# Kernel optimization log

Measured on AMD Instinct MI355X. Metric: run time of the kernel, lower is better.

The kernel has to match this reference:

```python
import jax, jax.numpy as jnp
import numpy as np
import math

D_MODEL = 1024
NUM_HEADS = 16
HEAD_DIM = D_MODEL // NUM_HEADS
ROPE_BASE = 10000.0
ROTARY_DIM = HEAD_DIM - HEAD_DIM % 2  # 64


def setup_inputs() -> dict:
    key = jax.random.key(0)
    ks = jax.random.split(key, 6)
    B, T = 4, 2048
    tokens = jax.random.normal(ks[0], (B, T, D_MODEL), dtype=jnp.float32)
    padding_mask = jax.random.randint(ks[1], (B, T), 0, 2) == 1  # True = pad
    s = 1.0 / math.sqrt(D_MODEL)
    W_qkv = jax.random.normal(ks[2], (D_MODEL, 3 * D_MODEL), dtype=jnp.float32) * s
    b_qkv = jnp.zeros((3 * D_MODEL,), dtype=jnp.float32)
    W_out = jax.random.normal(ks[3], (D_MODEL, D_MODEL), dtype=jnp.float32) * s
    b_out = jnp.zeros((D_MODEL,), dtype=jnp.float32)
    return {"tokens": tokens, "padding_mask": padding_mask,
            "W_qkv": W_qkv, "b_qkv": b_qkv, "W_out": W_out, "b_out": b_out}


def _apply_rope(x):
    # x: [B, H, T, head_dim]; full head dim is rotary here (ROTARY_DIM == HEAD_DIM)
    T = x.shape[-2]
    pos = jnp.arange(T, dtype=jnp.float32)[:, None]                      # [T,1]
    freqs = jnp.exp(jnp.arange(0, ROTARY_DIM, 2, dtype=jnp.float32)
                    * (-math.log(ROPE_BASE) / ROTARY_DIM))               # [rd/2]
    ang = pos * freqs[None, :]                                           # [T, rd/2]
    sin = jnp.sin(ang)[None, None].astype(x.dtype)
    cos = jnp.cos(ang)[None, None].astype(x.dtype)
    rot = x[..., :ROTARY_DIM].reshape(*x.shape[:-1], ROTARY_DIM // 2, 2)
    even, odd = rot[..., 0], rot[..., 1]
    rotated = jnp.stack((even * cos - odd * sin, even * sin + odd * cos), axis=-1)
    rotated = rotated.reshape(*x.shape[:-1], ROTARY_DIM)
    return jnp.concatenate([rotated, x[..., ROTARY_DIM:]], axis=-1)


def _safe_key_padding_mask(padding_mask):
    # True = pad; if a row is fully padded, unmask it to avoid NaN softmax rows
    all_pad = jnp.all(padding_mask, axis=-1, keepdims=True)
    return jnp.where(all_pad, False, padding_mask)


def reference(tokens, padding_mask, W_qkv, b_qkv, W_out, b_out):
    B, T, _ = tokens.shape
    qkv = tokens @ W_qkv + b_qkv                                         # [B,T,3d]
    q, k, v = jnp.split(qkv, 3, axis=-1)
    def split_heads(x):
        return x.reshape(B, T, NUM_HEADS, HEAD_DIM).transpose(0, 2, 1, 3)
    q, k, v = split_heads(q), split_heads(k), split_heads(v)
    q = _apply_rope(q)
    k = _apply_rope(k)
    valid = ~_safe_key_padding_mask(padding_mask)                        # [B,T], True = attend
    scores = jnp.einsum('bhqd,bhkd->bhqk', q, k) / math.sqrt(HEAD_DIM)   # [B,H,T,T]
    neg = jnp.asarray(jnp.finfo(scores.dtype).min, scores.dtype)
    scores = jnp.where(valid[:, None, None, :], scores, neg)
    attn = jax.nn.softmax(scores, axis=-1)
    out = jnp.einsum('bhqk,bhkd->bhqd', attn, v)                         # [B,H,T,hd]
    out = out.transpose(0, 2, 1, 3).reshape(B, T, D_MODEL)
    return out @ W_out + b_out
```

## Files before the change

### kernel.cpp

```cpp
#include <hip/hip_runtime.h>
#include <cmath>

#define T_SEQ 2048
#define NH    16
#define HD    64
#define DM    1024
#define BATCH 4

typedef __attribute__((ext_vector_type(8))) short s16x8;
typedef __attribute__((ext_vector_type(8))) _Float16 f16x8;
typedef __attribute__((ext_vector_type(2))) __fp16 fp16v2;
typedef __attribute__((ext_vector_type(4))) float f32x4;
typedef unsigned short ushort_t;

__device__ __forceinline__ ushort_t f2h(float x) {
    union { _Float16 h; ushort_t u; } v; v.h = (_Float16)x; return v.u;
}
__device__ __forceinline__ float h2f(ushort_t u) {
    union { ushort_t u; _Float16 h; } v; v.u = u; return (float)v.h;
}
__device__ __forceinline__ float exp2_raw(float x) {
    return __builtin_amdgcn_exp2f(x);
}
__device__ __forceinline__ unsigned pkrtz(float a, float b) {
    union { fp16v2 h; unsigned u; } v;
    v.h = __builtin_amdgcn_cvt_pkrtz(a, b);
    return v.u;
}

__device__ __forceinline__ void dma16(const void* g, const void* l) {
    __builtin_amdgcn_global_load_lds(
        (const __attribute__((address_space(1))) unsigned int*)(unsigned long long)g,
        (__attribute__((address_space(3))) unsigned int*)(unsigned int)(unsigned long long)l,
        16, 0, 0);
}

__global__ void maskprep_kernel(const int* __restrict__ pad, float* __restrict__ valid)
{
    __shared__ int sall[256];
    const int b = blockIdx.x;
    const int t = threadIdx.x;
    int allp = 1;
    for (int i = t; i < T_SEQ; i += 256) allp &= (pad[b*T_SEQ + i] != 0) ? 1 : 0;
    sall[t] = allp;
    __syncthreads();
    for (int s = 128; s > 0; s >>= 1) {
        if (t < s) sall[t] &= sall[t + s];
        __syncthreads();
    }
    const int ap = sall[0];
    for (int i = t; i < T_SEQ; i += 256) {
        const int p = (pad[b*T_SEQ + i] != 0) ? 1 : 0;
        valid[b*T_SEQ + i] = (p && !ap) ? -1e30f : 0.0f;
    }
}

__global__ __launch_bounds__(256)
void transpose_split_kernel(const float* __restrict__ W,
                            ushort_t* __restrict__ Th, ushort_t* __restrict__ Tl,
                            int K, int N)
{
    __shared__ float T[64][68];
    const int tid = threadIdx.x;
    const int n0 = blockIdx.x * 64;
    const int k0 = blockIdx.y * 64;
#pragma unroll
    for (int i = 0; i < 4; ++i) {
        const int kr = (tid >> 4) + i*16;
        const int nc = (tid & 15) * 4;
        const float4 v = *(const float4*)&W[(size_t)(k0 + kr)*N + n0 + nc];
        T[nc+0][kr] = v.x; T[nc+1][kr] = v.y; T[nc+2][kr] = v.z; T[nc+3][kr] = v.w;
    }
    __syncthreads();
#pragma unroll
    for (int i = 0; i < 4; ++i) {
        const int nr = (tid >> 4) + i*16;
        const int kc = (tid & 15) * 4;
        ushort_t h[4], l[4];
#pragma unroll
        for (int j = 0; j < 4; ++j) {
            const float x = T[nr][kc + j] * 32.0f;
            h[j] = f2h(x);
            l[j] = f2h(x - h2f(h[j]));
        }
        const size_t off = (size_t)(n0 + nr)*K + k0 + kc;
        *(short4*)&Th[off] = make_short4((short)h[0], (short)h[1], (short)h[2], (short)h[3]);
        *(short4*)&Tl[off] = make_short4((short)l[0], (short)l[1], (short)l[2], (short)l[3]);
    }
}

__global__ __launch_bounds__(256)
void split_kernel(const float* __restrict__ X, ushort_t* __restrict__ H)
{
    const int i = blockIdx.x * 256 + threadIdx.x;
    const float4 v = ((const float4*)X)[i];
    *(short4*)&H[(size_t)i*4] = make_short4(
        (short)f2h(v.x), (short)f2h(v.y), (short)f2h(v.z), (short)f2h(v.w));
}

template<int EPI>
__global__ __launch_bounds__(256)
void mfma_gemm_kernel(const ushort_t* __restrict__ Atf,
                      const ushort_t* __restrict__ BTh, const ushort_t* __restrict__ BTl,
                      const float* __restrict__ bias,
                      float* __restrict__ O0,
                      ushort_t* __restrict__ Qf,
                      ushort_t* __restrict__ Khf,
                      ushort_t* __restrict__ Vthf,
                      int M, int N, int K)
{
    __shared__ __align__(16) char smem[34816];
    char* smA  = smem;
    char* smBh = smem + 4096;
    char* smBl = smem + 12288;

    const int tid  = threadIdx.x;
    const int w    = tid >> 6;
    const int ln   = tid & 63;
    const int lx   = ln & 15;
    const int quad = ln >> 4;
    const int mw   = (w >> 1) * 32;
    const int nw   = (w & 1) * 64;
    const int m0   = blockIdx.y * 64;
    const int n0   = blockIdx.x * 128;

    const int swc = ((ln & 3) ^ ((ln >> 3) & 3)) * 8;
    const size_t gaA = (size_t)(m0 + w*16 + (ln >> 2))*K + swc;
    const size_t gaB = (size_t)(n0 + w*32 + (ln >> 2))*K + swc;
    const int ldsA = (w*64 + ln)*16;
    const int ldsB = (w*128 + ln)*16;

#define ISSUE_DMA(kk) do {                                               \
        dma16(Atf + gaA + (kk),        smA  + ldsA);                     \
        dma16(BTh + gaB + (kk),        smBh + ldsB);                     \
        dma16(BTh + gaB + 16*K + (kk), smBh + ldsB + 1024);              \
        dma16(BTl + gaB + (kk),        smBl + ldsB);                     \
        dma16(BTl + gaB + 16*K + (kk), smBl + ldsB + 1024);              \
    } while (0)

    f32x4 acc[2][4];
#pragma unroll
    for (int mt = 0; mt < 2; ++mt)
#pragma unroll
        for (int nt = 0; nt < 4; ++nt) acc[mt][nt] = (f32x4){0.f,0.f,0.f,0.f};

    ISSUE_DMA(0);

    const int cs = (quad ^ ((lx >> 1) & 3)) * 16;

    for (int kk = 0; kk < K; kk += 32) {
        __syncthreads();

        f16x8 bfh[4], bfl[4];
#pragma unroll
        for (int nt = 0; nt < 4; ++nt) {
            const int off = (nw + nt*16 + lx)*64 + cs;
            bfh[nt] = *(const f16x8*)(smBh + off);
            bfl[nt] = *(const f16x8*)(smBl + off);
        }
        f16x8 af0, af1;
        {
            af0 = *(const f16x8*)(smA + (mw + lx)*64 + cs);
            af1 = *(const f16x8*)(smA + (mw + 16 + lx)*64 + cs);
        }
        __syncthreads();
        if (kk + 32 < K) ISSUE_DMA(kk + 32);

        __builtin_amdgcn_s_setprio(1);
#pragma unroll
        for (int nt = 0; nt < 4; ++nt) {
            acc[0][nt] = __builtin_amdgcn_mfma_f32_16x16x32_f16(af0, bfh[nt], acc[0][nt], 0, 0, 0);
            acc[0][nt] = __builtin_amdgcn_mfma_f32_16x16x32_f16(af0, bfl[nt], acc[0][nt], 0, 0, 0);
        }
#pragma unroll
        for (int nt = 0; nt < 4; ++nt) {
            acc[1][nt] = __builtin_amdgcn_mfma_f32_16x16x32_f16(af1, bfh[nt], acc[1][nt], 0, 0, 0);
            acc[1][nt] = __builtin_amdgcn_mfma_f32_16x16x32_f16(af1, bfl[nt], acc[1][nt], 0, 0, 0);
        }
        __builtin_amdgcn_s_setprio(0);
    }
#undef ISSUE_DMA

    const float INV32 = 0.03125f;
    if (EPI == 0) {
#pragma unroll
        for (int nt = 0; nt < 4; ++nt) {
            const int n = n0 + nw + nt*16 + lx;
#pragma unroll
            for (int mt = 0; mt < 2; ++mt)
#pragma unroll
                for (int r = 0; r < 4; ++r) {
                    const int m = m0 + mw + mt*16 + quad*4 + r;
                    O0[(size_t)m*N + n] = acc[mt][nt][r]*INV32 + bias[n];
                }
        }
    } else {
        const int which = n0 >> 10;
        const int hbase = (n0 & 1023) >> 6;
        const int b     = m0 >> 11;
        const int t0    = m0 & 2047;
        float* Ct = (float*)smem;
        const float ssign = (lx & 1) ? 1.0f : -1.0f;

        __syncthreads();
        if (which < 2) {
#pragma unroll
            for (int nt = 0; nt < 4; ++nt) {
                const int nl = nw + nt*16 + lx;
                const int d  = nl & 63;
                const float bn = bias[n0 + nl];
                const float freq = expf(-(float)(d >> 1) * 0.28782313662425575f);
#pragma unroll
                for (int mt = 0; mt < 2; ++mt)
#pragma unroll
                    for (int r = 0; r < 4; ++r) {
                        const int ml = mw + mt*16 + quad*4 + r;
                        const int t  = t0 + ml;
                        float res = acc[mt][nt][r]*INV32 + bn;
                        const float ang = (float)t * freq;
                        const float sn = sinf(ang), cs2 = cosf(ang);
                        const float prt = __shfl_xor(res, 1);
                        res = res*cs2 + ssign*prt*sn;
                        if (which == 0) res *= 0.18033688011112042f;
                        Ct[ml*132 + nl] = res;
                    }
            }
        } else {
#pragma unroll
            for (int nt = 0; nt < 4; ++nt) {
                const int nl = nw + nt*16 + lx;
                const float bn = bias[n0 + nl];
#pragma unroll
                for (int mt = 0; mt < 2; ++mt)
#pragma unroll
                    for (int r = 0; r < 4; ++r) {
                        const int ml = mw + mt*16 + quad*4 + r;
                        Ct[nl*68 + ml] = acc[mt][nt][r]*INV32 + bn;
                    }
            }
        }
        __syncthreads();

        if (which < 2) {
#pragma unroll
            for (int u = 0; u < 4; ++u) {
                const int L  = u*32 + (tid >> 3);
                const int t  = L & 63;
                const int hl = L >> 6;
                const int dg = (tid & 7) * 8;
                const float* src = &Ct[t*132 + hl*64 + dg];
                float v[8];
                *(f32x4*)&v[0] = *(const f32x4*)src;
                *(f32x4*)&v[4] = *(const f32x4*)(src + 4);
                s16x8 h8;
#pragma unroll
                for (int j = 0; j < 8; ++j) h8[j] = (short)f2h(v[j]);
                const int bh = b*NH + hbase + hl;
                const size_t off = (((size_t)bh)*T_SEQ + t0 + t)*64 + dg;
                if (which == 0) *(s16x8*)&Qf [off] = h8;
                else            *(s16x8*)&Khf[off] = h8;
            }
        } else {
#pragma unroll
            for (int u = 0; u < 4; ++u) {
                const int row = u*32 + (tid >> 3);
                const int d   = row & 63;
                const int hl  = row >> 6;
                const int tg  = (tid & 7) * 8;
                const float* src = &Ct[row*68 + tg];
                float v[8];
                *(f32x4*)&v[0] = *(const f32x4*)src;
                *(f32x4*)&v[4] = *(const f32x4*)(src + 4);
                s16x8 h8;
#pragma unroll
                for (int j = 0; j < 8; ++j) h8[j] = (short)f2h(v[j]);
                const int bh = b*NH + hbase + hl;
                const size_t off = (((size_t)bh)*HD + d)*T_SEQ + t0 + tg;
                *(s16x8*)&Vthf[off] = h8;
            }
        }
    }
}

__global__ __launch_bounds__(256, 3)
void attn_mfma_kernel(const ushort_t* __restrict__ Qf,
                      const ushort_t* __restrict__ Khf,
                      const ushort_t* __restrict__ Vthf,
                      const float* __restrict__ mbias,
                      ushort_t* __restrict__ AOf)
{
    __shared__ ushort_t KH[64*64];
    __shared__ ushort_t VH[64*64];
    __shared__ float    MB[T_SEQ];

    const int tid  = threadIdx.x;
    const int w    = tid >> 6;
    const int ln   = tid & 63;
    const int lx   = ln & 15;
    const int quad = ln >> 4;

    const int id = blockIdx.x;
    const int qt = (id >> 3) & 15;
    const int bh = ((id >> 7) << 3) | (id & 7);
    const int b  = bh >> 4;
    const int h  = bh & 15;
    const int qrow0 = qt*128 + w*32;

    f16x8 qf[2][2];
#pragma unroll
    for (int qb = 0; qb < 2; ++qb) {
        const size_t qo = (((size_t)bh)*T_SEQ + qrow0 + qb*16 + lx)*HD + quad*8;
        qf[qb][0] = *(const f16x8*)&Qf[qo];
        qf[qb][1] = *(const f16x8*)&Qf[qo + 32];
    }

    {
        const f32x4* msrc = (const f32x4*)(mbias + (size_t)b*T_SEQ);
        f32x4* mdst = (f32x4*)MB;
#pragma unroll
        for (int i = 0; i < 2; ++i) mdst[tid + i*256] = msrc[tid + i*256];
    }

    const int sj   = ln >> 3;
    const int sch  = ln & 7;
    const int srow = w*16 + sj;
    const size_t kg0 = ((size_t)bh*T_SEQ + srow)*HD + sch*8;
    const size_t vg0 = ((size_t)bh*HD + srow)*T_SEQ + sch*8;
    const int lw0 = srow*64 + ((sch ^ (sj & 3)) << 3);
    const int lw1 = (srow + 8)*64 + ((sch ^ (sj & 3) ^ 4) << 3);

    const int r0  = ((lx >> 2) << 3) + (lx & 3);
    const int ka0 = r0*64 + ((quad ^ (lx & 7)) << 3);
    const int gv  = (lx & 3) ^ (((lx >> 3) & 1) << 2);
    const int va0 = lx*64 + ((quad ^ gv) << 3);

    f32x4 o[2][4];
#pragma unroll
    for (int qb = 0; qb < 2; ++qb)
#pragma unroll
        for (int nt = 0; nt < 4; ++nt) o[qb][nt] = (f32x4){0.f, 0.f, 0.f, 0.f};
    float mrun[2] = {-INFINITY, -INFINITY};
    float lrun[2] = {0.f, 0.f};

    s16x8 rkh0, rkh1, rvh0, rvh1;
    rkh0 = *(const s16x8*)&Khf [kg0];
    rkh1 = *(const s16x8*)&Khf [kg0 + (size_t)8*HD];
    rvh0 = *(const s16x8*)&Vthf[vg0];
    rvh1 = *(const s16x8*)&Vthf[vg0 + (size_t)8*T_SEQ];
    *(s16x8*)&KH[lw0] = rkh0;  *(s16x8*)&KH[lw1] = rkh1;
    *(s16x8*)&VH[lw0] = rvh0;  *(s16x8*)&VH[lw1] = rvh1;
    __syncthreads();

    for (int kt = 0; kt < T_SEQ/64; ++kt) {
        const int ktn = (kt+1 < T_SEQ/64) ? kt+1 : kt;
        const size_t kgt = kg0 + (size_t)ktn*64*HD;
        const size_t vgt = vg0 + ktn*64;
        rkh0 = *(const s16x8*)&Khf [kgt];
        rkh1 = *(const s16x8*)&Khf [kgt + (size_t)8*HD];
        rvh0 = *(const s16x8*)&Vthf[vgt];
        rvh1 = *(const s16x8*)&Vthf[vgt + (size_t)8*T_SEQ];

        f32x4 mb[4];
#pragma unroll
        for (int nt = 0; nt < 4; ++nt)
            mb[nt] = *(const f32x4*)&MB[kt*64 + (quad << 3) + ((nt >> 1) << 5) + ((nt & 1) << 2)];

        f32x4 s[2][4];
        __builtin_amdgcn_s_setprio(1);
#pragma unroll
        for (int nt = 0; nt < 4; ++nt) {
            const int a0 = ka0 + ((nt & 1) << 8) + ((nt >> 1) << 11);
            const f16x8 kh0 = *(const f16x8*)&KH[a0];
            const f16x8 kh1 = *(const f16x8*)&KH[a0 ^ 32];
            s[0][nt] = mb[nt];
            s[1][nt] = mb[nt];
            s[0][nt] = __builtin_amdgcn_mfma_f32_16x16x32_f16(kh0, qf[0][0], s[0][nt], 0, 0, 0);
            s[0][nt] = __builtin_amdgcn_mfma_f32_16x16x32_f16(kh1, qf[0][1], s[0][nt], 0, 0, 0);
            s[1][nt] = __builtin_amdgcn_mfma_f32_16x16x32_f16(kh0, qf[1][0], s[1][nt], 0, 0, 0);
            s[1][nt] = __builtin_amdgcn_mfma_f32_16x16x32_f16(kh1, qf[1][1], s[1][nt], 0, 0, 0);
        }
        __builtin_amdgcn_s_setprio(0);

        float mt[2];
#pragma unroll
        for (int qb = 0; qb < 2; ++qb) {
            const float m0q = fmaxf(fmaxf(s[qb][0][0], s[qb][0][1]), fmaxf(s[qb][0][2], s[qb][0][3]));
            const float m1q = fmaxf(fmaxf(s[qb][1][0], s[qb][1][1]), fmaxf(s[qb][1][2], s[qb][1][3]));
            const float m2q = fmaxf(fmaxf(s[qb][2][0], s[qb][2][1]), fmaxf(s[qb][2][2], s[qb][2][3]));
            const float m3q = fmaxf(fmaxf(s[qb][3][0], s[qb][3][1]), fmaxf(s[qb][3][2], s[qb][3][3]));
            float m = fmaxf(fmaxf(m0q, m1q), fmaxf(m2q, m3q));
            m = fmaxf(m, __shfl_xor(m, 16));
            m = fmaxf(m, __shfl_xor(m, 32));
            mt[qb] = m;
        }

        const bool stable = (mt[0] - mrun[0] <= 8.0f) && (mt[1] - mrun[1] <= 8.0f);
        if (!__all(stable)) {
#pragma unroll
            for (int qb = 0; qb < 2; ++qb) {
                const float mnew  = fmaxf(mrun[qb], mt[qb]);
                const float alpha = exp2_raw(mrun[qb] - mnew);
                mrun[qb] = mnew;
                lrun[qb] *= alpha;
                float ar[4];
#pragma unroll
                for (int r = 0; r < 4; ++r)
                    ar[r] = __shfl(alpha, (ln & 48) | ((quad << 2) + r));
#pragma unroll
                for (int nt = 0; nt < 4; ++nt)
#pragma unroll
                    for (int r = 0; r < 4; ++r) o[qb][nt][r] *= ar[r];
            }
        }

        union PU { unsigned u[4]; f16x8 v; };
        PU pf[2][2];
#pragma unroll
        for (int qb = 0; qb < 2; ++qb) {
            float lt = 0.f;
#pragma unroll
            for (int nt = 0; nt < 4; ++nt)
#pragma unroll
                for (int r = 0; r < 4; ++r) {
                    s[qb][nt][r] = exp2_raw(s[qb][nt][r] - mrun[qb]);
                    lt += s[qb][nt][r];
                }
            lrun[qb] += lt;

            pf[qb][0].u[0] = pkrtz(s[qb][0][0], s[qb][0][1]);
            pf[qb][0].u[1] = pkrtz(s[qb][0][2], s[qb][0][3]);
            pf[qb][0].u[2] = pkrtz(s[qb][1][0], s[qb][1][1]);
            pf[qb][0].u[3] = pkrtz(s[qb][1][2], s[qb][1][3]);
            pf[qb][1].u[0] = pkrtz(s[qb][2][0], s[qb][2][1]);
            pf[qb][1].u[1] = pkrtz(s[qb][2][2], s[qb][2][3]);
            pf[qb][1].u[2] = pkrtz(s[qb][3][0], s[qb][3][1]);
            pf[qb][1].u[3] = pkrtz(s[qb][3][2], s[qb][3][3]);
        }

        __builtin_amdgcn_s_setprio(1);
#pragma unroll
        for (int nt = 0; nt < 4; ++nt) {
            const int v0 = va0 + (nt << 10);
            const f16x8 vh0 = *(const f16x8*)&VH[v0];
            const f16x8 vh1 = *(const f16x8*)&VH[v0 ^ 32];
            o[0][nt] = __builtin_amdgcn_mfma_f32_16x16x32_f16(pf[0][0].v, vh0, o[0][nt], 0, 0, 0);
            o[0][nt] = __builtin_amdgcn_mfma_f32_16x16x32_f16(pf[0][1].v, vh1, o[0][nt], 0, 0, 0);
            o[1][nt] = __builtin_amdgcn_mfma_f32_16x16x32_f16(pf[1][0].v, vh0, o[1][nt], 0, 0, 0);
            o[1][nt] = __builtin_amdgcn_mfma_f32_16x16x32_f16(pf[1][1].v, vh1, o[1][nt], 0, 0, 0);
        }
        __builtin_amdgcn_s_setprio(0);

        __syncthreads();
        *(s16x8*)&KH[lw0] = rkh0;  *(s16x8*)&KH[lw1] = rkh1;
        *(s16x8*)&VH[lw0] = rvh0;  *(s16x8*)&VH[lw1] = rvh1;
        __syncthreads();
    }

#pragma unroll
    for (int qb = 0; qb < 2; ++qb) {
        lrun[qb] += __shfl_xor(lrun[qb], 16);
        lrun[qb] += __shfl_xor(lrun[qb], 32);
        const float linv = 1.0f / lrun[qb];
        float ir[4];
#pragma unroll
        for (int r = 0; r < 4; ++r)
            ir[r] = __shfl(linv, (ln & 48) | ((quad << 2) + r));
#pragma unroll
        for (int nt = 0; nt < 4; ++nt)
#pragma unroll
            for (int r = 0; r < 4; ++r) {
                const int t = qrow0 + qb*16 + quad*4 + r;
                const float res = o[qb][nt][r] * ir[r];
                const size_t off = (((size_t)b)*T_SEQ + t)*DM + h*HD + nt*16 + lx;
                AOf[off] = f2h(res);
            }
    }
}

extern "C" void kernel_launch(void* const* d_in, const int* in_sizes, int n_in,
                              void* d_out, int out_size, void* d_ws, size_t ws_size,
                              hipStream_t stream)
{
    const float* tokens = (const float*)d_in[0];
    const int*   pad    = (const int*)d_in[1];
    const float* Wqkv   = (const float*)d_in[2];
    const float* bqkv   = (const float*)d_in[3];
    const float* Wout   = (const float*)d_in[4];
    const float* bout   = (const float*)d_in[5];
    float* out = (float*)d_out;

    const size_t SZ = (size_t)8388608;
    ushort_t* U = (ushort_t*)d_ws;
    ushort_t* Qf   = U;
    ushort_t* Khf  = U + SZ;
    ushort_t* Vthf = U + 2*SZ;
    float* MSK = (float*)(U + 6*SZ);
    ushort_t* R   = (ushort_t*)(MSK + 8192);
    ushort_t* WqkvTh = R;
    ushort_t* WqkvTl = R + (size_t)3*DM*DM;
    ushort_t* AOf = R;
    ushort_t* TokF = (ushort_t*)d_out;
    ushort_t* WoutTh = Khf;
    ushort_t* WoutTl = Khf + (size_t)DM*DM;

    maskprep_kernel<<<dim3(BATCH), dim3(256), 0, stream>>>(pad, MSK);
    split_kernel<<<dim3(8192), dim3(256), 0, stream>>>(tokens, TokF);
    transpose_split_kernel<<<dim3(48, 16), dim3(256), 0, stream>>>(
        Wqkv, WqkvTh, WqkvTl, DM, 3*DM);
    mfma_gemm_kernel<1><<<dim3(24, 128), dim3(256), 0, stream>>>(
        TokF, WqkvTh, WqkvTl, bqkv, nullptr,
        Qf, Khf, Vthf, BATCH*T_SEQ, 3*DM, DM);
    attn_mfma_kernel<<<dim3(1024), dim3(256), 0, stream>>>(
        Qf, Khf, Vthf, MSK, AOf);
    transpose_split_kernel<<<dim3(16, 16), dim3(256), 0, stream>>>(
        Wout, WoutTh, WoutTl, DM, DM);
    mfma_gemm_kernel<0><<<dim3(8, 128), dim3(256), 0, stream>>>(
        AOf, WoutTh, WoutTl, bout, out,
        nullptr, nullptr, nullptr, BATCH*T_SEQ, DM, DM);
}
```

Baseline: 393.5 us.

## Drop low-half weight split in GEMMs and double-buffer LDS tiles

After: 331.4 us. 1.19x faster.

```diff
diff --git a/kernel.cpp b/kernel.cpp
--- a/kernel.cpp
+++ b/kernel.cpp
@@ -56,9 +56,8 @@
 }
 
 __global__ __launch_bounds__(256)
-void transpose_split_kernel(const float* __restrict__ W,
-                            ushort_t* __restrict__ Th, ushort_t* __restrict__ Tl,
-                            int K, int N)
+void transpose_h_kernel(const float* __restrict__ W,
+                        ushort_t* __restrict__ Th, int K, int N)
 {
     __shared__ float T[64][68];
     const int tid = threadIdx.x;
@@ -76,16 +75,11 @@
     for (int i = 0; i < 4; ++i) {
         const int nr = (tid >> 4) + i*16;
         const int kc = (tid & 15) * 4;
-        ushort_t h[4], l[4];
-#pragma unroll
-        for (int j = 0; j < 4; ++j) {
-            const float x = T[nr][kc + j] * 32.0f;
-            h[j] = f2h(x);
-            l[j] = f2h(x - h2f(h[j]));
-        }
+        ushort_t h[4];
+#pragma unroll
+        for (int j = 0; j < 4; ++j) h[j] = f2h(T[nr][kc + j] * 32.0f);
         const size_t off = (size_t)(n0 + nr)*K + k0 + kc;
         *(short4*)&Th[off] = make_short4((short)h[0], (short)h[1], (short)h[2], (short)h[3]);
-        *(short4*)&Tl[off] = make_short4((short)l[0], (short)l[1], (short)l[2], (short)l[3]);
     }
 }
 
@@ -101,7 +95,7 @@
 template<int EPI>
 __global__ __launch_bounds__(256)
 void mfma_gemm_kernel(const ushort_t* __restrict__ Atf,
-                      const ushort_t* __restrict__ BTh, const ushort_t* __restrict__ BTl,
+                      const ushort_t* __restrict__ BTh,
                       const float* __restrict__ bias,
                       float* __restrict__ O0,
                       ushort_t* __restrict__ Qf,
@@ -110,9 +104,10 @@
                       int M, int N, int K)
 {
     __shared__ __align__(16) char smem[34816];
-    char* smA  = smem;
-    char* smBh = smem + 4096;
-    char* smBl = smem + 12288;
+    char* smA0 = smem;
+    char* smA1 = smem + 4096;
+    char* smB0 = smem + 8192;
+    char* smB1 = smem + 16384;
 
     const int tid  = threadIdx.x;
     const int w    = tid >> 6;
@@ -130,12 +125,10 @@
     const int ldsA = (w*64 + ln)*16;
     const int ldsB = (w*128 + ln)*16;
 
-#define ISSUE_DMA(kk) do {                                               \
-        dma16(Atf + gaA + (kk),        smA  + ldsA);                     \
-        dma16(BTh + gaB + (kk),        smBh + ldsB);                     \
-        dma16(BTh + gaB + 16*K + (kk), smBh + ldsB + 1024);              \
-        dma16(BTl + gaB + (kk),        smBl + ldsB);                     \
-        dma16(BTl + gaB + 16*K + (kk), smBl + ldsB + 1024);              \
+#define ISSUE_DMA(kk, dA, dB) do {                                       \
+        dma16(Atf + gaA + (kk),        (dA) + ldsA);                     \
+        dma16(BTh + gaB + (kk),        (dB) + ldsB);                     \
+        dma16(BTh + gaB + 16*K + (kk), (dB) + ldsB + 1024);              \
     } while (0)
 
     f32x4 acc[2][4];
@@ -144,41 +137,33 @@
 #pragma unroll
         for (int nt = 0; nt < 4; ++nt) acc[mt][nt] = (f32x4){0.f,0.f,0.f,0.f};
 
-    ISSUE_DMA(0);
-
     const int cs = (quad ^ ((lx >> 1) & 3)) * 16;
 
-    for (int kk = 0; kk < K; kk += 32) {
-        __syncthreads();
-
-        f16x8 bfh[4], bfl[4];
-#pragma unroll
-        for (int nt = 0; nt < 4; ++nt) {
-            const int off = (nw + nt*16 + lx)*64 + cs;
-            bfh[nt] = *(const f16x8*)(smBh + off);
-            bfl[nt] = *(const f16x8*)(smBl + off);
-        }
-        f16x8 af0, af1;
-        {
-            af0 = *(const f16x8*)(smA + (mw + lx)*64 + cs);
-            af1 = *(const f16x8*)(smA + (mw + 16 + lx)*64 + cs);
-        }
-        __syncthreads();
-        if (kk + 32 < K) ISSUE_DMA(kk + 32);
-
-        __builtin_amdgcn_s_setprio(1);
-#pragma unroll
-        for (int nt = 0; nt < 4; ++nt) {
-            acc[0][nt] = __builtin_amdgcn_mfma_f32_16x16x32_f16(af0, bfh[nt], acc[0][nt], 0, 0, 0);
-            acc[0][nt] = __builtin_amdgcn_mfma_f32_16x16x32_f16(af0, bfl[nt], acc[0][nt], 0, 0, 0);
-        }
-#pragma unroll
-        for (int nt = 0; nt < 4; ++nt) {
-            acc[1][nt] = __builtin_amdgcn_mfma_f32_16x16x32_f16(af1, bfh[nt], acc[1][nt], 0, 0, 0);
-            acc[1][nt] = __builtin_amdgcn_mfma_f32_16x16x32_f16(af1, bfl[nt], acc[1][nt], 0, 0, 0);
-        }
-        __builtin_amdgcn_s_setprio(0);
-    }
+#define GEMM_STEP(kk, cA, cB, nA, nB) do {                                \
+        if ((kk) + 32 < K) ISSUE_DMA((kk) + 32, nA, nB);                  \
+        f16x8 bfh[4];                                                     \
+        _Pragma("unroll")                                                 \
+        for (int nt = 0; nt < 4; ++nt)                                    \
+            bfh[nt] = *(const f16x8*)((cB) + (nw + nt*16 + lx)*64 + cs);  \
+        const f16x8 af0 = *(const f16x8*)((cA) + (mw + lx)*64 + cs);      \
+        const f16x8 af1 = *(const f16x8*)((cA) + (mw + 16 + lx)*64 + cs); \
+        __builtin_amdgcn_s_setprio(1);                                    \
+        _Pragma("unroll")                                                 \
+        for (int nt = 0; nt < 4; ++nt) {                                  \
+            acc[0][nt] = __builtin_amdgcn_mfma_f32_16x16x32_f16(af0, bfh[nt], acc[0][nt], 0, 0, 0); \
+            acc[1][nt] = __builtin_amdgcn_mfma_f32_16x16x32_f16(af1, bfh[nt], acc[1][nt], 0, 0, 0); \
+        }                                                                 \
+        __builtin_amdgcn_s_setprio(0);                                    \
+        __syncthreads();                                                  \
+    } while (0)
+
+    ISSUE_DMA(0, smA0, smB0);
+    __syncthreads();
+    for (int kk = 0; kk < K; kk += 64) {
+        GEMM_STEP(kk,      smA0, smB0, smA1, smB1);
+        GEMM_STEP(kk + 32, smA1, smB1, smA0, smB0);
+    }
+#undef GEMM_STEP
 #undef ISSUE_DMA
 
     const float INV32 = 0.03125f;
@@ -497,24 +482,22 @@
     float* MSK = (float*)(U + 6*SZ);
     ushort_t* R   = (ushort_t*)(MSK + 8192);
     ushort_t* WqkvTh = R;
-    ushort_t* WqkvTl = R + (size_t)3*DM*DM;
     ushort_t* AOf = R;
     ushort_t* TokF = (ushort_t*)d_out;
     ushort_t* WoutTh = Khf;
-    ushort_t* WoutTl = Khf + (size_t)DM*DM;
 
     maskprep_kernel<<<dim3(BATCH), dim3(256), 0, stream>>>(pad, MSK);
     split_kernel<<<dim3(8192), dim3(256), 0, stream>>>(tokens, TokF);
-    transpose_split_kernel<<<dim3(48, 16), dim3(256), 0, stream>>>(
-        Wqkv, WqkvTh, WqkvTl, DM, 3*DM);
+    transpose_h_kernel<<<dim3(48, 16), dim3(256), 0, stream>>>(
+        Wqkv, WqkvTh, DM, 3*DM);
     mfma_gemm_kernel<1><<<dim3(24, 128), dim3(256), 0, stream>>>(
-        TokF, WqkvTh, WqkvTl, bqkv, nullptr,
+        TokF, WqkvTh, bqkv, nullptr,
         Qf, Khf, Vthf, BATCH*T_SEQ, 3*DM, DM);
     attn_mfma_kernel<<<dim3(1024), dim3(256), 0, stream>>>(
         Qf, Khf, Vthf, MSK, AOf);
-    transpose_split_kernel<<<dim3(16, 16), dim3(256), 0, stream>>>(
-        Wout, WoutTh, WoutTl, DM, DM);
+    transpose_h_kernel<<<dim3(16, 16), dim3(256), 0, stream>>>(
+        Wout, WoutTh, DM, DM);
     mfma_gemm_kernel<0><<<dim3(8, 128), dim3(256), 0, stream>>>(
-        AOf, WoutTh, WoutTl, bout, out,
+        AOf, WoutTh, bout, out,
         nullptr, nullptr, nullptr, BATCH*T_SEQ, DM, DM);
 }
```
